# Kernel optimization log

Measured on AMD Instinct MI355X. Metric: run time of the kernel, lower is better.

The kernel has to match this reference:

```python
import jax, jax.numpy as jnp
import numpy as np

N, IN, HID, Z = 96, 64, 256, 64
TRI = N * (N + 1) // 2
MPM_ITERS = 50


def setup_inputs() -> dict:
    key = jax.random.key(0)
    ks = jax.random.split(key, 24)
    w = lambda k, s: jax.random.normal(k, s, jnp.float32) * 0.05
    x = jax.random.normal(ks[0], (N, IN), jnp.float32)
    edge_index = jax.random.randint(ks[1], (2, 2048), 0, N)
    batch = jnp.zeros((N,), jnp.int32)
    # symmetric binary adjacency with self-loops (ground truth graph)
    U = (jax.random.uniform(ks[2], (N, N)) < 0.15).astype(jnp.float32)
    Au = jnp.triu(U, 1)
    A_gt = Au + Au.T + jnp.eye(N, dtype=jnp.float32)
    return dict(
        x=x, edge_index=edge_index, batch=batch, A_gt=A_gt,
        conv1_w=w(ks[3], (IN, HID)), conv1_b=jnp.zeros((HID,)),
        bn1_g=jnp.ones((HID,)), bn1_b=jnp.zeros((HID,)),
        conv2_w=w(ks[4], (HID, HID)), conv2_b=jnp.zeros((HID,)),
        bn2_g=jnp.ones((HID,)), bn2_b=jnp.zeros((HID,)),
        mu_w=w(ks[5], (HID, Z)), mu_b=jnp.zeros((Z,)),
        lv_w=w(ks[6], (HID, Z)), lv_b=jnp.zeros((Z,)),
        dec1_w=w(ks[7], (Z, HID)), dec1_b=jnp.zeros((HID,)),
        dec2_w=w(ks[8], (HID, TRI)), dec2_b=jnp.zeros((TRI,)),
        eps=jax.random.normal(ks[9], (1, Z), jnp.float32),
    )


def _gcn(h, W, b, src, dst, n):
    # PyG GCNConv: add self-loops, sym-normalized aggregation
    h = h @ W
    sl = jnp.arange(n)
    s = jnp.concatenate([src, sl])
    d = jnp.concatenate([dst, sl])
    deg = jnp.zeros((n,), h.dtype).at[d].add(1.0)
    dis = jax.lax.rsqrt(deg)
    coef = (dis[s] * dis[d])[:, None]
    return jnp.zeros_like(h).at[d].add(h[s] * coef) + b


def _bn(h, g, b):
    m = h.mean(0)
    v = h.var(0)
    return (h - m) * jax.lax.rsqrt(v + 1e-5) * g + b


def reference(x, edge_index, batch, A_gt, conv1_w, conv1_b, bn1_g, bn1_b,
              conv2_w, conv2_b, bn2_g, bn2_b, mu_w, mu_b, lv_w, lv_b,
              dec1_w, dec1_b, dec2_w, dec2_b, eps):
    n = A_gt.shape[0]
    src, dst = edge_index[0], edge_index[1]
    h = jax.nn.relu(_bn(_gcn(x, conv1_w, conv1_b, src, dst, n), bn1_g, bn1_b))
    h = jax.nn.relu(_bn(_gcn(h, conv2_w, conv2_b, src, dst, n), bn2_g, bn2_b))
    g = jax.ops.segment_sum(h, batch, num_segments=1)           # sum pool, batch=1
    mu = g @ mu_w + mu_b
    lv = g @ lv_w + lv_b
    z = mu + eps * jnp.exp(0.5 * lv)                            # reparam
    vec = (jax.nn.relu(z @ dec1_w + dec1_b) @ dec2_w + dec2_b)[0]  # (TRI,)
    iu = jnp.triu_indices(n)
    adj = jnp.zeros((n, n), vec.dtype).at[iu].set(vec)
    logits_adj = adj + adj.T - jnp.diag(jnp.diag(adj))
    B = jax.nn.sigmoid(logits_adj)
    degA = A_gt.sum(1)
    degB = jax.lax.stop_gradient(B.sum(1))                      # .detach() in torch
    # --- vectorized _edge_sim_tensor: S[i,j,a,b] (N^4) ---
    Ad, Bd = jnp.diag(A_gt), jnp.diag(B)
    off = 1.0 - jnp.eye(n, dtype=vec.dtype)
    P = A_gt * Ad[:, None] * Ad[None, :] * off                  # zero where i==j
    Q = B * Bd[:, None] * Bd[None, :] * off                     # zero where a==b
    S = P[:, :, None, None] * Q[None, None, :, :]
    D = Ad[:, None] * Bd[None, :] / (jnp.abs(degA[:, None] - degB[None, :]) + 1.0)
    ii = jnp.arange(n)
    S = S.at[ii[:, None], ii[:, None], ii[None, :], ii[None, :]].set(D)
    # --- vectorized MPM (max-pooling matching), 50 iterations ---
    def body(_, xm):
        T = jnp.max(S * xm[None, :, None, :], axis=3)           # max_b x[j,b]*S[i,j,a,b]
        msg = jnp.sum(T * off[:, :, None], axis=1)              # sum over j != i
        xn = xm * D + msg
        return xn / jnp.linalg.norm(xn)
    X = jax.lax.fori_loop(0, MPM_ITERS, body, jnp.full((n, n), 1.0 / n, vec.dtype))
    # scipy.linear_sum_assignment on a square matrix returns row_ind = arange(N),
    # and the torch code permutes A_gt by `row` only => A_perm == A_gt.
    tri_truth = A_gt[iu]
    rec = jnp.mean(jnp.maximum(vec, 0.0) - vec * tri_truth + jnp.log1p(jnp.exp(-jnp.abs(vec))))
    kl = -0.5 * jnp.mean(1.0 + lv - mu * mu - jnp.exp(lv))
    return rec + kl, X
```

## Files before the change

kernel.cpp:

```cpp
#include <hip/hip_runtime.h>
#include <cmath>

#define Nn 96
#define NB 32
#define NT 512
#define GT (NB*NT)
#define MAXD 40
#define NE 2048
#define TRIN 4656
#define NITER 50
#define SPIN_CAP (1 << 22)
#define AGENT __HIP_MEMORY_SCOPE_AGENT

enum {
  OFF_FLAGS = 0,
  OFF_POOL  = 32,
  OFF_VEC   = 288,
  OFF_XW    = 4944,
  OFF_H1    = 29520,
  OFF_X0    = 54096,
  OFF_X1    = 63312,
  OFF_X2    = 72528,
  WS_END    = 81744
};

__device__ __forceinline__ int tri_idx(int i, int j) {
  return i * Nn - (i * (i - 1)) / 2 + (j - i);
}

__device__ __forceinline__ float gload(const float* p) {
  return __hip_atomic_load(p, __ATOMIC_RELAXED, AGENT);
}
__device__ __forceinline__ void gstore(float* p, float v) {
  __hip_atomic_store(p, v, __ATOMIC_RELAXED, AGENT);
}
__device__ __forceinline__ void gload2(const float* p, float& x, float& y) {
  unsigned long long u =
      __hip_atomic_load((const unsigned long long*)p, __ATOMIC_RELAXED, AGENT);
  union { unsigned long long u; float f[2]; } c; c.u = u;
  x = c.f[0]; y = c.f[1];
}

__device__ __forceinline__ void gbar(int* flags, int target) {
  asm volatile("s_waitcnt vmcnt(0)" ::: "memory");
  __syncthreads();
  if (threadIdx.x == 0)
    __hip_atomic_store(&flags[blockIdx.x], target, __ATOMIC_RELAXED, AGENT);
  if (threadIdx.x < NB)
    while (__hip_atomic_load(&flags[threadIdx.x], __ATOMIC_RELAXED, AGENT) < target) {}
  __syncthreads();
}

__device__ __forceinline__ float wsum64(float v) {
  #pragma unroll
  for (int m = 32; m >= 1; m >>= 1) v += __shfl_xor(v, m, 64);
  return v;
}

__global__ __launch_bounds__(NT)
void k_fused(const float* x, const int* ei, const float* A,
             const float* w1, const float* b1, const float* g1, const float* be1,
             const float* w2, const float* b2, const float* g2, const float* be2,
             const float* muw, const float* mub, const float* lvw, const float* lvb,
             const float* d1w, const float* d1b, const float* d2w, const float* d2b,
             const float* eps, float* ws, float* out) {
  __shared__ float SBIG[Nn * 97];
  __shared__ float SAUX[768];
  __shared__ float SAUX2[768];
  __shared__ float Qsh[3 * Nn];
  __shared__ float Msh[3 * Nn];
  __shared__ float partM[12 * Nn];
  __shared__ float red[NT];
  __shared__ float degl[Nn];
  __shared__ float DEGAl[Nn];
  __shared__ float Bdsh[Nn];
  __shared__ float DegBsh[4];
  __shared__ float mv[16];
  __shared__ float sc[4];
  __shared__ unsigned char nbr[Nn * MAXD];
  __shared__ int ncnt[Nn];

  const int tid  = threadIdx.x;
  const int bid  = blockIdx.x;
  const int gtid = bid * NT + tid;
  const int a0   = bid * 3;
  int* flags = (int*)ws;
  int bt = 0;

  for (int o = tid; o < Nn * 97; o += NT) SBIG[o] = 0.f;
  if (tid < Nn) degl[tid] = 0.f;
  __syncthreads();
  for (int e = tid; e < NE; e += NT) atomicAdd(&degl[ei[NE + e]], 1.f);
  if (tid < Nn) atomicAdd(&degl[tid], 1.f);
  __syncthreads();
  for (int e = tid; e < NE; e += NT) {
    int s = ei[e], d = ei[NE + e];
    float c = (1.f / sqrtf(degl[s])) * (1.f / sqrtf(degl[d]));
    atomicAdd(&SBIG[d * 97 + s], c);
  }
  if (tid < Nn) atomicAdd(&SBIG[tid * 97 + tid], 1.f / degl[tid]);
  if (tid < Nn) {
    float s = 0.f;
    for (int j = 0; j < Nn; ++j) s += A[tid * Nn + j];
    DEGAl[tid] = s;
    int cnt = 0;
    for (int j = 0; j < Nn; ++j)
      if (j != tid && A[tid * Nn + j] != 0.f && cnt < MAXD)
        nbr[tid * MAXD + cnt++] = (unsigned char)j;
    ncnt[tid] = cnt;
  }
  {
    if (tid < 192) SAUX[tid] = x[a0 * 64 + tid];
    __syncthreads();
    for (int o = tid; o < 3 * 256; o += NT) {
      int rl = o >> 8, c = o & 255;
      float s = 0.f;
      #pragma unroll 8
      for (int k = 0; k < 64; ++k) s += SAUX[rl * 64 + k] * w1[k * 256 + c];
      gstore(&ws[OFF_XW + (a0 + rl) * 256 + c], s);
    }
  }
  gbar(flags, ++bt);

  {
    const int c0 = bid * 8;
    for (int o = tid; o < 768; o += NT) {
      int cl = o / Nn, k = o - cl * Nn;
      SAUX[o] = gload(&ws[OFF_XW + k * 256 + c0 + cl]);
    }
    __syncthreads();
    for (int o = tid; o < 768; o += NT) {
      int cl = o / Nn, r = o - cl * Nn;
      float s = b1[c0 + cl];
      #pragma unroll 8
      for (int k = 0; k < Nn; ++k) s += SBIG[r * 97 + k] * SAUX[cl * Nn + k];
      SAUX2[cl * Nn + r] = s;
    }
    __syncthreads();
    if (tid < 8) {
      float m = 0.f;
      for (int r = 0; r < Nn; ++r) m += SAUX2[tid * Nn + r];
      m /= (float)Nn;
      float v = 0.f;
      for (int r = 0; r < Nn; ++r) { float d = SAUX2[tid * Nn + r] - m; v += d * d; }
      v /= (float)Nn;
      mv[tid * 2] = m; mv[tid * 2 + 1] = 1.f / sqrtf(v + 1e-5f);
    }
    __syncthreads();
    for (int o = tid; o < 768; o += NT) {
      int cl = o / Nn, r = o - cl * Nn; int c = c0 + cl;
      float y = (SAUX2[o] - mv[cl * 2]) * mv[cl * 2 + 1] * g1[c] + be1[c];
      gstore(&ws[OFF_H1 + r * 256 + c], fmaxf(y, 0.f));
    }
  }
  gbar(flags, ++bt);

  {
    for (int o = tid; o < 768; o += NT)
      SAUX[o] = gload(&ws[OFF_H1 + a0 * 256 + o]);
    __syncthreads();
    for (int o = tid; o < 768; o += NT) {
      int rl = o >> 8, c = o & 255;
      float s = 0.f;
      #pragma unroll 4
      for (int k = 0; k < 256; ++k) s += SAUX[rl * 256 + k] * w2[k * 256 + c];
      gstore(&ws[OFF_XW + (a0 + rl) * 256 + c], s);
    }
  }
  gbar(flags, ++bt);

  {
    const int c0 = bid * 8;
    for (int o = tid; o < 768; o += NT) {
      int cl = o / Nn, k = o - cl * Nn;
      SAUX[o] = gload(&ws[OFF_XW + k * 256 + c0 + cl]);
    }
    __syncthreads();
    for (int o = tid; o < 768; o += NT) {
      int cl = o / Nn, r = o - cl * Nn;
      float s = b2[c0 + cl];
      #pragma unroll 8
      for (int k = 0; k < Nn; ++k) s += SBIG[r * 97 + k] * SAUX[cl * Nn + k];
      SAUX2[cl * Nn + r] = s;
    }
    __syncthreads();
    if (tid < 8) {
      int c = c0 + tid;
      float m = 0.f;
      for (int r = 0; r < Nn; ++r) m += SAUX2[tid * Nn + r];
      m /= (float)Nn;
      float v = 0.f;
      for (int r = 0; r < Nn; ++r) { float d = SAUX2[tid * Nn + r] - m; v += d * d; }
      v /= (float)Nn;
      float rs = 1.f / sqrtf(v + 1e-5f);
      float gg = g2[c], bb = be2[c], p = 0.f;
      for (int r = 0; r < Nn; ++r)
        p += fmaxf((SAUX2[tid * Nn + r] - m) * rs * gg + bb, 0.f);
      gstore(&ws[OFF_POOL + c], p);
    }
  }
  gbar(flags, ++bt);

  if (tid < 288) {
    gstore(&ws[OFF_X0 + a0 * 96 + tid], -1.f);
    gstore(&ws[OFF_X1 + a0 * 96 + tid], -1.f);
    gstore(&ws[OFF_X2 + a0 * 96 + tid], -1.f);
  }
  if (tid < 256) SAUX[tid] = gload(&ws[OFF_POOL + tid]);
  __syncthreads();
  if (tid < 64) {
    float mu = mub[tid], lv = lvb[tid];
    for (int k = 0; k < 256; ++k) {
      float g = SAUX[k];
      mu += g * muw[k * 64 + tid];
      lv += g * lvw[k * 64 + tid];
    }
    SAUX2[tid] = mu; SAUX2[64 + tid] = lv;
    SAUX2[128 + tid] = mu + eps[tid] * expf(0.5f * lv);
  }
  __syncthreads();
  if (tid < 256) {
    float s = d1b[tid];
    for (int k = 0; k < 64; ++k) s += SAUX2[128 + k] * d1w[k * 256 + tid];
    SAUX[256 + tid] = fmaxf(s, 0.f);
  } else if (bid == 0 && tid == 256) {
    float s = 0.f;
    for (int t = 0; t < 64; ++t) {
      float mu = SAUX2[t], lv = SAUX2[64 + t];
      s += 1.f + lv - mu * mu - expf(lv);
    }
    sc[1] = -0.5f * s / 64.f;
  }
  __syncthreads();
  {
    int c = bid * 146 + tid;
    if (tid < 146 && c < TRIN) {
      float s = d2b[c];
      #pragma unroll 4
      for (int k = 0; k < 256; ++k) s += SAUX[256 + k] * d2w[k * TRIN + c];
      gstore(&ws[OFF_VEC + c], s);
    }
  }
  gbar(flags, ++bt);

  for (int o = tid; o < TRIN; o += NT) SBIG[o] = gload(&ws[OFF_VEC + o]);
  __syncthreads();
  if (tid < Nn) Bdsh[tid] = 1.f / (1.f + expf(-SBIG[tri_idx(tid, tid)]));
  __syncthreads();
  if (tid < 288) {
    int cl = tid / 96, b = tid - cl * 96, a = a0 + cl;
    int i_ = a < b ? a : b, j_ = a < b ? b : a;
    float s_ = 1.f / (1.f + expf(-SBIG[tri_idx(i_, j_)]));
    partM[cl * 96 + b] = s_;
    Qsh[cl * 96 + b] = (a == b) ? 0.f : s_ * Bdsh[a] * Bdsh[b];
  }
  __syncthreads();
  if (tid < 3) {
    float s = 0.f;
    for (int b = 0; b < Nn; ++b) s += partM[tid * 96 + b];
    DegBsh[tid] = s;
  }
  __syncthreads();
  float Dreg = 0.f;
  if (tid < 288) {
    int cl = tid / 96, i = tid - cl * 96;
    Dreg = Bdsh[a0 + cl] / (fabsf(DEGAl[i] - DegBsh[cl]) + 1.f);
  }
  if (bid == 0) {
    float s = 0.f;
    for (int i = 0; i < Nn; ++i)
      for (int j = i + tid; j < Nn; j += NT) {
        float v = SBIG[tri_idx(i, j)];
        float tt = A[i * Nn + j];
        s += fmaxf(v, 0.f) - v * tt + log1pf(expf(-fabsf(v)));
      }
    red[tid] = s;
    __syncthreads();
    for (int st = 256; st >= 1; st >>= 1) { if (tid < st) red[tid] += red[tid + st]; __syncthreads(); }
    if (tid == 0) out[0] = red[0] / (float)TRIN + sc[1];
  }
  if (tid < 288) gstore(&ws[OFF_X2 + a0 * 96 + tid], 1.f / (float)Nn);
  __syncthreads();

  float* pr = ws + OFF_X2;
  float* ps = ws + OFF_X1;
  float* pw = ws + OFF_X0;

  for (int it = 0; it < NITER; ++it) {
    float vx[9], vy[9]; int base[9];
    #pragma unroll
    for (int k = 0; k < 9; ++k) {
      int o2 = k * NT + tid;
      int a = o2 / 48, r = o2 - a * 48;
      base[k] = a * 96 + 2 * r;
      gload2(pr + base[k], vx[k], vy[k]);
    }
    #pragma unroll
    for (int k = 0; k < 9; ++k) {
      int guard = 0;
      while (fminf(vx[k], vy[k]) <= 0.f && ++guard < SPIN_CAP)
        gload2(pr + base[k], vx[k], vy[k]);
    }
    float ls = 0.f;
    #pragma unroll
    for (int k = 0; k < 9; ++k) {
      int o2 = k * NT + tid; int a = o2 / 48;
      int xi = base[k] + a;
      SBIG[xi] = vx[k]; SBIG[xi + 1] = vy[k];
      ls += vx[k] * vx[k] + vy[k] * vy[k];
    }
    if (tid < 288) gstore(ps + a0 * 96 + tid, -1.f);
    ls = wsum64(ls);
    if ((tid & 63) == 0) red[tid >> 6] = ls;
    __syncthreads();
    const float nrm = sqrtf(red[0] + red[1] + red[2] + red[3] +
                            red[4] + red[5] + red[6] + red[7]);

    if (tid < 4 * Nn) {
      int bseg = tid / Nn, j = tid - bseg * Nn;
      int b0 = bseg * 24;
      float m0 = 0.f, m1 = 0.f, m2 = 0.f;
      #pragma unroll
      for (int bb = 0; bb < 24; ++bb) {
        float xv = SBIG[(b0 + bb) * 97 + j];
        m0 = fmaxf(m0, Qsh[b0 + bb] * xv);
        m1 = fmaxf(m1, Qsh[Nn + b0 + bb] * xv);
        m2 = fmaxf(m2, Qsh[2 * Nn + b0 + bb] * xv);
      }
      partM[(bseg * 3 + 0) * Nn + j] = m0;
      partM[(bseg * 3 + 1) * Nn + j] = m1;
      partM[(bseg * 3 + 2) * Nn + j] = m2;
    }
    __syncthreads();
    if (tid < 3 * Nn) {
      int cl = tid / Nn, j = tid - cl * Nn;
      Msh[tid] = fmaxf(fmaxf(partM[cl * Nn + j], partM[(3 + cl) * Nn + j]),
                       fmaxf(partM[(6 + cl) * Nn + j], partM[(9 + cl) * Nn + j]));
    }
    __syncthreads();

    float val = 0.f;
    if (tid < 288) {
      int cl = tid / 96, i = tid - cl * 96;
      float s = 0.f;
      int nc = ncnt[i];
      for (int k = 0; k < nc; ++k) s += Msh[cl * Nn + nbr[i * MAXD + k]];
      float xo = SBIG[(a0 + cl) * 97 + i];
      val = fmaxf((xo * Dreg + s) / nrm, 1e-30f);
    }
    asm volatile("s_waitcnt vmcnt(0)" ::: "memory");
    if (tid < 288) gstore(pw + a0 * 96 + tid, val);
    __syncthreads();
    float* t_ = pr; pr = pw; pw = ps; ps = t_;
  }

  if (bid != 0) return;
  {
    float vx[9], vy[9]; int base[9];
    #pragma unroll
    for (int k = 0; k < 9; ++k) {
      int o2 = k * NT + tid;
      int a = o2 / 48, r = o2 - a * 48;
      base[k] = a * 96 + 2 * r;
      gload2(pr + base[k], vx[k], vy[k]);
    }
    #pragma unroll
    for (int k = 0; k < 9; ++k) {
      int guard = 0;
      while (fminf(vx[k], vy[k]) <= 0.f && ++guard < SPIN_CAP)
        gload2(pr + base[k], vx[k], vy[k]);
    }
    float ls = 0.f;
    #pragma unroll
    for (int k = 0; k < 9; ++k) ls += vx[k] * vx[k] + vy[k] * vy[k];
    ls = wsum64(ls);
    if ((tid & 63) == 0) red[tid >> 6] = ls;
    __syncthreads();
    const float nrm = sqrtf(red[0] + red[1] + red[2] + red[3] +
                            red[4] + red[5] + red[6] + red[7]);
    #pragma unroll
    for (int k = 0; k < 9; ++k) {
      int o2 = k * NT + tid;
      int a = o2 / 48, i0 = 2 * (o2 - a * 48);
      out[1 + i0 * 96 + a] = vx[k] / nrm;
      out[1 + (i0 + 1) * 96 + a] = vy[k] / nrm;
    }
  }
}

extern "C" void kernel_launch(void* const* d_in, const int* in_sizes, int n_in,
                              void* d_out, int out_size, void* d_ws, size_t ws_size,
                              hipStream_t stream) {
  const float* x   = (const float*)d_in[0];
  const int*   ei  = (const int*)d_in[1];
  const float* A   = (const float*)d_in[3];
  const float* w1  = (const float*)d_in[4];
  const float* b1  = (const float*)d_in[5];
  const float* g1  = (const float*)d_in[6];
  const float* be1 = (const float*)d_in[7];
  const float* w2  = (const float*)d_in[8];
  const float* b2  = (const float*)d_in[9];
  const float* g2  = (const float*)d_in[10];
  const float* be2 = (const float*)d_in[11];
  const float* muw = (const float*)d_in[12];
  const float* mub = (const float*)d_in[13];
  const float* lvw = (const float*)d_in[14];
  const float* lvb = (const float*)d_in[15];
  const float* d1w = (const float*)d_in[16];
  const float* d1b = (const float*)d_in[17];
  const float* d2w = (const float*)d_in[18];
  const float* d2b = (const float*)d_in[19];
  const float* eps = (const float*)d_in[20];
  float* ws  = (float*)d_ws;
  float* out = (float*)d_out;

  hipMemsetAsync(ws, 0, NB * sizeof(int), stream);

  k_fused<<<dim3(NB), dim3(NT), 0, stream>>>(
      x, ei, A, w1, b1, g1, be1, w2, b2, g2, be2,
      muw, mub, lvw, lvb, d1w, d1b, d2w, d2b, eps, ws, out);
}
```

Before: 474.7 us.

## Fuse first GCN matmul per block, drop a grid barrier, pair stores

Each block now computes its own 8-column slice of x@W1 for all 96 rows straight from global inputs, instead of computing 3 rows, publishing them to the workspace and waiting at a grid-wide barrier. This removes one global barrier and a workspace round trip in exchange for redundant reads of x. The MPM loop now publishes its flag-carrying values as 64-bit paired stores, using a lane shuffle to pair neighbouring results. The spin-wait is restructured to poll all 9 pending pairs together rather than one after another.

```diff
diff --git a/kernel.cpp b/kernel.cpp
--- a/kernel.cpp
+++ b/kernel.cpp
@@ -4,12 +4,11 @@
 #define Nn 96
 #define NB 32
 #define NT 512
-#define GT (NB*NT)
 #define MAXD 40
 #define NE 2048
 #define TRIN 4656
 #define NITER 50
-#define SPIN_CAP (1 << 22)
+#define SPIN_CAP (1 << 20)
 #define AGENT __HIP_MEMORY_SCOPE_AGENT
 
 enum {
@@ -39,6 +38,10 @@
       __hip_atomic_load((const unsigned long long*)p, __ATOMIC_RELAXED, AGENT);
   union { unsigned long long u; float f[2]; } c; c.u = u;
   x = c.f[0]; y = c.f[1];
+}
+__device__ __forceinline__ void gstore2(float* p, float a, float b) {
+  union { unsigned long long u; float f[2]; } c; c.f[0] = a; c.f[1] = b;
+  __hip_atomic_store((unsigned long long*)p, c.u, __ATOMIC_RELAXED, AGENT);
 }
 
 __device__ __forceinline__ void gbar(int* flags, int target) {
@@ -75,15 +78,14 @@
   __shared__ float DEGAl[Nn];
   __shared__ float Bdsh[Nn];
   __shared__ float DegBsh[4];
-  __shared__ float mv[16];
   __shared__ float sc[4];
   __shared__ unsigned char nbr[Nn * MAXD];
   __shared__ int ncnt[Nn];
 
-  const int tid  = threadIdx.x;
-  const int bid  = blockIdx.x;
-  const int gtid = bid * NT + tid;
-  const int a0   = bid * 3;
+  const int tid = threadIdx.x;
+  const int bid = blockIdx.x;
+  const int a0  = bid * 3;
+  const int c0  = bid * 8;
   int* flags = (int*)ws;
   int bt = 0;
 
@@ -109,47 +111,34 @@
         nbr[tid * MAXD + cnt++] = (unsigned char)j;
     ncnt[tid] = cnt;
   }
-  {
-    if (tid < 192) SAUX[tid] = x[a0 * 64 + tid];
-    __syncthreads();
-    for (int o = tid; o < 3 * 256; o += NT) {
-      int rl = o >> 8, c = o & 255;
-      float s = 0.f;
-      #pragma unroll 8
-      for (int k = 0; k < 64; ++k) s += SAUX[rl * 64 + k] * w1[k * 256 + c];
-      gstore(&ws[OFF_XW + (a0 + rl) * 256 + c], s);
-    }
-  }
-  gbar(flags, ++bt);
-
-  {
-    const int c0 = bid * 8;
-    for (int o = tid; o < 768; o += NT) {
-      int cl = o / Nn, k = o - cl * Nn;
-      SAUX[o] = gload(&ws[OFF_XW + k * 256 + c0 + cl]);
-    }
-    __syncthreads();
-    for (int o = tid; o < 768; o += NT) {
-      int cl = o / Nn, r = o - cl * Nn;
-      float s = b1[c0 + cl];
-      #pragma unroll 8
-      for (int k = 0; k < Nn; ++k) s += SBIG[r * 97 + k] * SAUX[cl * Nn + k];
-      SAUX2[cl * Nn + r] = s;
-    }
-    __syncthreads();
-    if (tid < 8) {
-      float m = 0.f;
-      for (int r = 0; r < Nn; ++r) m += SAUX2[tid * Nn + r];
-      m /= (float)Nn;
-      float v = 0.f;
-      for (int r = 0; r < Nn; ++r) { float d = SAUX2[tid * Nn + r] - m; v += d * d; }
-      v /= (float)Nn;
-      mv[tid * 2] = m; mv[tid * 2 + 1] = 1.f / sqrtf(v + 1e-5f);
-    }
-    __syncthreads();
-    for (int o = tid; o < 768; o += NT) {
-      int cl = o / Nn, r = o - cl * Nn; int c = c0 + cl;
-      float y = (SAUX2[o] - mv[cl * 2]) * mv[cl * 2 + 1] * g1[c] + be1[c];
+  for (int o = tid; o < 768; o += NT) {
+    int cl = o / Nn, k = o - cl * Nn;
+    float s = 0.f;
+    #pragma unroll 8
+    for (int kk = 0; kk < 64; ++kk) s += x[k * 64 + kk] * w1[kk * 256 + c0 + cl];
+    SAUX[o] = s;
+  }
+  __syncthreads();
+  for (int o = tid; o < 768; o += NT) {
+    int cl = o / Nn, r = o - cl * Nn;
+    float s = b1[c0 + cl];
+    #pragma unroll 8
+    for (int k = 0; k < Nn; ++k) s += SBIG[r * 97 + k] * SAUX[cl * Nn + k];
+    SAUX2[cl * Nn + r] = s;
+  }
+  __syncthreads();
+  if (tid < 8) {
+    int c = c0 + tid;
+    float m = 0.f;
+    for (int r = 0; r < Nn; ++r) m += SAUX2[tid * Nn + r];
+    m /= (float)Nn;
+    float v = 0.f;
+    for (int r = 0; r < Nn; ++r) { float d = SAUX2[tid * Nn + r] - m; v += d * d; }
+    v /= (float)Nn;
+    float rs = 1.f / sqrtf(v + 1e-5f);
+    float gg = g1[c], bb = be1[c];
+    for (int r = 0; r < Nn; ++r) {
+      float y = (SAUX2[tid * Nn + r] - m) * rs * gg + bb;
       gstore(&ws[OFF_H1 + r * 256 + c], fmaxf(y, 0.f));
     }
   }
@@ -170,7 +159,6 @@
   gbar(flags, ++bt);
 
   {
-    const int c0 = bid * 8;
     for (int o = tid; o < 768; o += NT) {
       int cl = o / Nn, k = o - cl * Nn;
       SAUX[o] = gload(&ws[OFF_XW + k * 256 + c0 + cl]);
@@ -201,10 +189,10 @@
   }
   gbar(flags, ++bt);
 
-  if (tid < 288) {
-    gstore(&ws[OFF_X0 + a0 * 96 + tid], -1.f);
-    gstore(&ws[OFF_X1 + a0 * 96 + tid], -1.f);
-    gstore(&ws[OFF_X2 + a0 * 96 + tid], -1.f);
+  if (tid < 288 && !(tid & 1)) {
+    gstore2(&ws[OFF_X0 + a0 * 96 + tid], -1.f, -1.f);
+    gstore2(&ws[OFF_X1 + a0 * 96 + tid], -1.f, -1.f);
+    gstore2(&ws[OFF_X2 + a0 * 96 + tid], -1.f, -1.f);
   }
   if (tid < 256) SAUX[tid] = gload(&ws[OFF_POOL + tid]);
   __syncthreads();
@@ -279,7 +267,8 @@
     for (int st = 256; st >= 1; st >>= 1) { if (tid < st) red[tid] += red[tid + st]; __syncthreads(); }
     if (tid == 0) out[0] = red[0] / (float)TRIN + sc[1];
   }
-  if (tid < 288) gstore(&ws[OFF_X2 + a0 * 96 + tid], 1.f / (float)Nn);
+  if (tid < 288 && !(tid & 1))
+    gstore2(&ws[OFF_X2 + a0 * 96 + tid], 1.f / (float)Nn, 1.f / (float)Nn);
   __syncthreads();
 
   float* pr = ws + OFF_X2;
@@ -295,11 +284,14 @@
       base[k] = a * 96 + 2 * r;
       gload2(pr + base[k], vx[k], vy[k]);
     }
-    #pragma unroll
-    for (int k = 0; k < 9; ++k) {
-      int guard = 0;
-      while (fminf(vx[k], vy[k]) <= 0.f && ++guard < SPIN_CAP)
-        gload2(pr + base[k], vx[k], vy[k]);
+    for (int guard = 0; guard < SPIN_CAP; ++guard) {
+      float mn = 1e30f;
+      #pragma unroll
+      for (int k = 0; k < 9; ++k) mn = fminf(mn, fminf(vx[k], vy[k]));
+      if (mn > 0.f) break;
+      #pragma unroll
+      for (int k = 0; k < 9; ++k)
+        if (fminf(vx[k], vy[k]) <= 0.f) gload2(pr + base[k], vx[k], vy[k]);
     }
     float ls = 0.f;
     #pragma unroll
@@ -309,7 +301,7 @@
       SBIG[xi] = vx[k]; SBIG[xi + 1] = vy[k];
       ls += vx[k] * vx[k] + vy[k] * vy[k];
     }
-    if (tid < 288) gstore(ps + a0 * 96 + tid, -1.f);
+    if (tid < 288 && !(tid & 1)) gstore2(ps + a0 * 96 + tid, -1.f, -1.f);
     ls = wsum64(ls);
     if ((tid & 63) == 0) red[tid >> 6] = ls;
     __syncthreads();
@@ -348,8 +340,9 @@
       float xo = SBIG[(a0 + cl) * 97 + i];
       val = fmaxf((xo * Dreg + s) / nrm, 1e-30f);
     }
+    float pvv = __shfl_xor(val, 1, 64);
     asm volatile("s_waitcnt vmcnt(0)" ::: "memory");
-    if (tid < 288) gstore(pw + a0 * 96 + tid, val);
+    if (tid < 288 && !(tid & 1)) gstore2(pw + a0 * 96 + tid, val, pvv);
     __syncthreads();
     float* t_ = pr; pr = pw; pw = ps; ps = t_;
   }
@@ -364,11 +357,14 @@
       base[k] = a * 96 + 2 * r;
       gload2(pr + base[k], vx[k], vy[k]);
     }
-    #pragma unroll
-    for (int k = 0; k < 9; ++k) {
-      int guard = 0;
-      while (fminf(vx[k], vy[k]) <= 0.f && ++guard < SPIN_CAP)
-        gload2(pr + base[k], vx[k], vy[k]);
+    for (int guard = 0; guard < SPIN_CAP; ++guard) {
+      float mn = 1e30f;
+      #pragma unroll
+      for (int k = 0; k < 9; ++k) mn = fminf(mn, fminf(vx[k], vy[k]));
+      if (mn > 0.f) break;
+      #pragma unroll
+      for (int k = 0; k < 9; ++k)
+        if (fminf(vx[k], vy[k]) <= 0.f) gload2(pr + base[k], vx[k], vy[k]);
     }
     float ls = 0.f;
     #pragma unroll
```

Result: no change. 472.5 us (-0.5%).
